# Kernel tuning notes

Measured on AMD Instinct MI355X. Metric: run time of the kernel, lower is better.

The kernel has to match this reference:

```python
import jax, jax.numpy as jnp
import numpy as np

HEAD_NUM = 16


def setup_inputs() -> dict:
    key = jax.random.key(0)
    k1, k2, k3, k4 = jax.random.split(key, 4)
    B, S, E = 8, 1024, 1024
    inputs = jax.random.normal(k1, (B, S, E), dtype=jnp.float32)
    W_Query = jax.random.normal(k2, (E, E), dtype=jnp.float32) * 0.05
    W_Key = jax.random.normal(k3, (E, E), dtype=jnp.float32) * 0.05
    W_Value = jax.random.normal(k4, (E, E), dtype=jnp.float32) * 0.05
    return {"inputs": inputs, "W_Query": W_Query, "W_Key": W_Key, "W_Value": W_Value}


def reference(inputs, W_Query, W_Key, W_Value):
    B, S, E = inputs.shape
    H = HEAD_NUM
    D = E // H
    # QKV projections: [B,S,E] @ [E,E] -> [B,S,E]
    q = jnp.einsum('bse,ef->bsf', inputs, W_Query).reshape(B, S, H, D)
    k = jnp.einsum('bse,ef->bsf', inputs, W_Key).reshape(B, S, H, D)
    v = jnp.einsum('bse,ef->bsf', inputs, W_Value).reshape(B, S, H, D)
    # NOTE: original has NO 1/sqrt(D) scaling.
    scores = jnp.einsum('bihd,bjhd->bhij', q, k)  # [B,H,S,S]
    att = jax.nn.softmax(scores, axis=-1)
    out = jnp.einsum('bhij,bjhd->bihd', att, v).reshape(B, S, E)
    return jax.nn.relu(out)
```

## Files before the change

### kernel.cpp

```cpp
#include <hip/hip_runtime.h>
#include <cstdint>
#include <cstddef>

#define B_ 8
#define S_ 1024
#define E_ 1024
#define H_ 16
#define D_ 64
#define M_ (B_*S_)

typedef _Float16 f16;
typedef __attribute__((ext_vector_type(8))) _Float16 f16x8;
typedef __attribute__((ext_vector_type(4))) _Float16 f16x4;
typedef __attribute__((ext_vector_type(4))) float  f32x4;
typedef __attribute__((ext_vector_type(16))) float f32x16;
typedef __attribute__((ext_vector_type(4))) int    int4v;
typedef __attribute__((ext_vector_type(2))) int    int2v;

__device__ __forceinline__ f32x4 mfma16(f16x8 a, f16x8 b, f32x4 c) {
  return __builtin_amdgcn_mfma_f32_16x16x32_f16(a, b, c, 0, 0, 0);
}
__device__ __forceinline__ f32x16 mfma32(f16x8 a, f16x8 b, f32x16 c) {
  return __builtin_amdgcn_mfma_f32_32x32x16_f16(a, b, c, 0, 0, 0);
}
__device__ __forceinline__ void gll16(const f16* g, f16* l) {
  __builtin_amdgcn_global_load_lds(
      (const __attribute__((address_space(1))) void*)g,
      (__attribute__((address_space(3))) void*)l, 16, 0, 0);
}
__device__ __forceinline__ int pkrtz(float lo, float hi) {
  return __builtin_bit_cast(int, __builtin_amdgcn_cvt_pkrtz(lo, hi));
}

__global__ __launch_bounds__(256) void prep_kernel(
    const float* __restrict__ X, const float* __restrict__ Wq,
    const float* __restrict__ Wk, const float* __restrict__ Wv,
    f16* __restrict__ Xf, f16* __restrict__ oq, f16* __restrict__ ok,
    f16* __restrict__ ov) {
  __shared__ float t[64][65];
  const int bid = blockIdx.x;
  if (bid < 4096) {
    size_t i = ((size_t)bid * 256 + threadIdx.x) * 8;
    f32x4 v0 = *(const f32x4*)&X[i];
    f32x4 v1 = *(const f32x4*)&X[i + 4];
    f16x8 hv;
#pragma unroll
    for (int j = 0; j < 4; ++j) {
      hv[j] = (f16)v0[j];
      hv[j + 4] = (f16)v1[j];
    }
    *(f16x8*)&Xf[i] = hv;
    return;
  }
  const int wid = bid - 4096;
  const int which = wid >> 8, tile = wid & 255;
  const float* W = which == 0 ? Wq : (which == 1 ? Wk : Wv);
  f16* o = which == 0 ? oq : (which == 1 ? ok : ov);
  const float scl = which == 0 ? 1.4426950408889634f : 1.0f;
  const int f0 = (tile & 15) * 64, e0 = (tile >> 4) * 64;
  const int tx = threadIdx.x & 63, tyy = threadIdx.x >> 6;
#pragma unroll
  for (int j = 0; j < 16; ++j) {
    int row = 4 * j + tyy;
    t[row][tx] = W[(size_t)(e0 + row) * E_ + f0 + tx];
  }
  __syncthreads();
#pragma unroll
  for (int j = 0; j < 16; ++j) {
    int row = 4 * j + tyy;
    o[(size_t)(f0 + row) * E_ + e0 + tx] = (f16)(t[tx][row] * scl);
  }
}

__global__ __launch_bounds__(256) void gemm_qkv_kernel(
    const f16* __restrict__ Xf,
    const f16* __restrict__ Wq, const f16* __restrict__ Wk,
    const f16* __restrict__ Wv,
    f16* __restrict__ Qf, f16* __restrict__ Kf, f16* __restrict__ Vt) {
  __shared__ f16 sA[128][64], sB[128][64];
  const int bid = blockIdx.x;
  const int xcd = bid & 7, idx = bid >> 3;
  const int mb = xcd * 8 + idx / 24;
  const int nb = idx % 24;
  const int z = nb >> 3;
  const int n0 = (nb & 7) * 128, m0 = mb * 128;
  const f16* __restrict__ Bt = z == 0 ? Wq : (z == 1 ? Wk : Wv);
  const int tid = threadIdx.x;
  const int lane = tid & 63, w = tid >> 6;
  const int wm = (w >> 1) * 64, wn = (w & 1) * 64;
  const int fr = lane & 15, fg = lane >> 4;
  f32x4 acc[4][4] = {};
  for (int k0 = 0; k0 < E_; k0 += 64) {
#pragma unroll
    for (int i = 0; i < 4; ++i) {
      int ci = tid + i * 256;
      int r = ci >> 3, cl = ci & 7;
      int cs = (cl ^ (r & 7)) * 8;
      gll16(Xf + (size_t)(m0 + r) * E_ + k0 + cs, &sA[0][0] + ci * 8);
      gll16(Bt + (size_t)(n0 + r) * E_ + k0 + cs, &sB[0][0] + ci * 8);
    }
    __syncthreads();
#pragma unroll
    for (int kh2 = 0; kh2 < 2; ++kh2) {
      f16x8 ah[4];
#pragma unroll
      for (int mi = 0; mi < 4; ++mi) {
        int rA = wm + mi * 16 + fr;
        ah[mi] = *(const f16x8*)&sA[rA][(((kh2 * 4 + fg) ^ (rA & 7))) * 8];
      }
#pragma unroll
      for (int ni = 0; ni < 4; ++ni) {
        int rB = wn + ni * 16 + fr;
        f16x8 bh = *(const f16x8*)&sB[rB][(((kh2 * 4 + fg) ^ (rB & 7))) * 8];
#pragma unroll
        for (int mi = 0; mi < 4; ++mi)
          acc[mi][ni] = mfma16(ah[mi], bh, acc[mi][ni]);
      }
    }
    __syncthreads();
  }
  if (z < 2) {
    f16* Of = z == 0 ? Qf : Kf;
#pragma unroll
    for (int mi = 0; mi < 4; ++mi)
#pragma unroll
      for (int ni = 0; ni < 4; ++ni)
#pragma unroll
        for (int r = 0; r < 4; ++r) {
          int row = m0 + wm + mi * 16 + (lane >> 4) * 4 + r;
          int col = n0 + wn + ni * 16 + fr;
          int bb = row >> 10, s = row & 1023;
          int hd = col >> 6, d = col & 63;
          Of[((size_t)(bb * H_ + hd) * S_ + s) * D_ + d] = (f16)acc[mi][ni][r];
        }
  } else {
#pragma unroll
    for (int mi = 0; mi < 4; ++mi)
#pragma unroll
      for (int ni = 0; ni < 4; ++ni) {
        int row = m0 + wm + mi * 16 + (lane >> 4) * 4;
        int col = n0 + wn + ni * 16 + fr;
        int bb = row >> 10, s = row & 1023;
        int hd = col >> 6, d = col & 63;
        f16x4 p;
#pragma unroll
        for (int r = 0; r < 4; ++r) p[r] = (f16)acc[mi][ni][r];
        *(f16x4*)&Vt[((size_t)(bb * H_ + hd) * D_ + d) * S_ + s] = p;
      }
  }
}

__global__ __launch_bounds__(256, 4) void attn_kernel(
    const f16* __restrict__ Qf, const f16* __restrict__ Kf,
    const f16* __restrict__ Vt, float* __restrict__ out) {
  __shared__ f16 sK[2][64][64], sV[2][64][64];
  const int bid = blockIdx.x;
  const int bh = (bid & 7) * 16 + (bid >> 6);
  const int qb = (bid >> 3) & 7;
  const int hd = bh & 15, bb = bh >> 4;
  const int tid = threadIdx.x;
  const int lane = tid & 63, w = tid >> 6;
  const int cq = lane & 31, h = lane >> 5;
  const int rsw = cq & 7;
  const size_t base = (size_t)bh * (S_ * D_);
  const f16* Qf_p = Qf + base;
  const f16* Kf_p = Kf + base;
  const f16* Vt_p = Vt + base;
  const int q0 = qb * 128 + w * 32;

  f16x8 qh_[4];
#pragma unroll
  for (int ks = 0; ks < 4; ++ks)
    qh_[ks] = *(const f16x8*)&Qf_p[(size_t)(q0 + cq) * D_ + ks * 16 + 8 * h];

  float m_run, l_run;
  f32x16 O[2] = {};
  f16x8 pf[4];

#define STAGE(buf, kb)                                                        \
  {                                                                           \
    _Pragma("unroll")                                                         \
    for (int half = 0; half < 2; ++half) {                                    \
      int ci = tid + half * 256;                                              \
      int row = ci >> 3, cl = ci & 7;                                         \
      int cs = cl ^ (row & 7);                                                \
      gll16(Kf_p + (size_t)((kb) + row) * D_ + cs * 8, &sK[buf][0][0] + ci * 8); \
      gll16(Vt_p + (size_t)row * S_ + (kb) + cs * 8, &sV[buf][0][0] + ci * 8);   \
    }                                                                         \
  }

#define QKT(scv, bufi)                                                        \
  {                                                                           \
    _Pragma("unroll")                                                         \
    for (int f = 0; f < 2; ++f) {                                             \
      _Pragma("unroll")                                                       \
      for (int ks = 0; ks < 4; ++ks) {                                        \
        int cc = ((2 * ks + h) ^ rsw) * 8;                                    \
        f16x8 kv = *(const f16x8*)&sK[bufi][f * 32 + cq][cc];                 \
        scv[f] = mfma32(kv, qh_[ks], scv[f]);                                 \
      }                                                                       \
    }                                                                         \
  }

#define MAXTREE(pm, scv)                                                      \
  {                                                                           \
    float t4[4];                                                              \
    _Pragma("unroll")                                                         \
    for (int i = 0; i < 4; ++i) {                                             \
      float a = fmaxf(fmaxf(scv[0][i], scv[0][i + 4]),                        \
                      fmaxf(scv[0][i + 8], scv[0][i + 12]));                  \
      float b = fmaxf(fmaxf(scv[1][i], scv[1][i + 4]),                        \
                      fmaxf(scv[1][i + 8], scv[1][i + 12]));                  \
      t4[i] = fmaxf(a, b);                                                    \
    }                                                                         \
    pm = fmaxf(fmaxf(t4[0], t4[1]), fmaxf(t4[2], t4[3]));                     \
    pm = fmaxf(pm, __shfl_xor(pm, 32));                                       \
  }

#define ROWSUM(rs, scv)                                                       \
  {                                                                           \
    float rs0 = 0.f, rs1 = 0.f, rs2 = 0.f, rs3 = 0.f;                         \
    _Pragma("unroll")                                                         \
    for (int f = 0; f < 2; ++f) {                                             \
      _Pragma("unroll")                                                       \
      for (int r4 = 0; r4 < 4; ++r4) {                                        \
        rs0 += scv[f][4 * r4 + 0];                                            \
        rs1 += scv[f][4 * r4 + 1];                                            \
        rs2 += scv[f][4 * r4 + 2];                                            \
        rs3 += scv[f][4 * r4 + 3];                                            \
      }                                                                       \
    }                                                                         \
    rs = (rs0 + rs1) + (rs2 + rs3);                                           \
    rs += __shfl_xor(rs, 32);                                                 \
  }

#define PFBUILD(scv)                                                          \
  {                                                                           \
    _Pragma("unroll")                                                         \
    for (int f = 0; f < 2; ++f) {                                             \
      _Pragma("unroll")                                                       \
      for (int ksl = 0; ksl < 2; ++ksl) {                                     \
        int b0 = 8 * ksl;                                                     \
        int a1 = pkrtz(scv[f][b0 + 0], scv[f][b0 + 1]);                       \
        int b1 = pkrtz(scv[f][b0 + 4], scv[f][b0 + 5]);                       \
        int2v r1 = __builtin_amdgcn_permlane32_swap(a1, b1, false, false);    \
        int a2 = pkrtz(scv[f][b0 + 2], scv[f][b0 + 3]);                       \
        int b2 = pkrtz(scv[f][b0 + 6], scv[f][b0 + 7]);                       \
        int2v r2 = __builtin_amdgcn_permlane32_swap(a2, b2, false, false);    \
        int4v wd;                                                             \
        wd[0] = r1[0]; wd[1] = r2[0]; wd[2] = r1[1]; wd[3] = r2[1];           \
        pf[2 * f + ksl] = __builtin_bit_cast(f16x8, wd);                      \
      }                                                                       \
    }                                                                         \
  }

#define PVT(bufi)                                                             \
  {                                                                           \
    _Pragma("unroll")                                                         \
    for (int ks = 0; ks < 4; ++ks) {                                          \
      int cc = ((2 * ks + h) ^ rsw) * 8;                                      \
      _Pragma("unroll")                                                       \
      for (int df = 0; df < 2; ++df) {                                        \
        f16x8 vf = *(const f16x8*)&sV[bufi][df * 32 + cq][cc];                \
        O[df] = mfma32(vf, pf[ks], O[df]);                                    \
      }                                                                       \
    }                                                                         \
  }

  STAGE(0, 0);
  asm volatile("s_waitcnt vmcnt(0)" ::: "memory");
  __builtin_amdgcn_sched_barrier(0);
  __builtin_amdgcn_s_barrier();
  STAGE(1, 64);
  {
    f32x16 sc[2] = {};
    __builtin_amdgcn_s_setprio(1);
    QKT(sc, 0);
    __builtin_amdgcn_s_setprio(0);
    float pm;
    MAXTREE(pm, sc);
    m_run = pm;
#pragma unroll
    for (int f = 0; f < 2; ++f)
#pragma unroll
      for (int r = 0; r < 16; ++r)
        sc[f][r] = __builtin_amdgcn_exp2f(sc[f][r] - pm);
    float rs;
    ROWSUM(rs, sc);
    l_run = rs;
    PFBUILD(sc);
    __builtin_amdgcn_s_setprio(1);
    PVT(0);
    __builtin_amdgcn_s_setprio(0);
  }
  asm volatile("s_waitcnt vmcnt(0)" ::: "memory");
  __builtin_amdgcn_sched_barrier(0);
  __builtin_amdgcn_s_barrier();

  for (int t = 1; t < 16; ++t) {
    const int cur = t & 1;
    if (t < 15) STAGE(cur ^ 1, (t + 1) * 64);

    f32x16 sc[2];
#pragma unroll
    for (int f = 0; f < 2; ++f)
#pragma unroll
      for (int r = 0; r < 16; ++r) sc[f][r] = -m_run;
    __builtin_amdgcn_s_setprio(1);
    QKT(sc, cur);
    __builtin_amdgcn_s_setprio(0);

#pragma unroll
    for (int f = 0; f < 2; ++f)
#pragma unroll
      for (int r = 0; r < 16; ++r)
        sc[f][r] = __builtin_amdgcn_exp2f(sc[f][r]);

    float pm;
    MAXTREE(pm, sc);
    if (__any(pm > 2048.f)) {
      float pmx = fmaxf(pm, 1.0f);
      float scl = 1.0f / pmx;
      m_run += __builtin_amdgcn_logf(pmx);
      l_run *= scl;
#pragma unroll
      for (int f = 0; f < 2; ++f)
#pragma unroll
        for (int r = 0; r < 16; ++r) sc[f][r] *= scl;
#pragma unroll
      for (int df = 0; df < 2; ++df)
#pragma unroll
        for (int i = 0; i < 16; ++i) O[df][i] *= scl;
    }

    float rs;
    ROWSUM(rs, sc);
    l_run += rs;
    PFBUILD(sc);
    __builtin_amdgcn_s_setprio(1);
    PVT(cur);
    __builtin_amdgcn_s_setprio(0);

    asm volatile("s_waitcnt vmcnt(0)" ::: "memory");
    __builtin_amdgcn_sched_barrier(0);
    __builtin_amdgcn_s_barrier();
  }

  float inv = 1.0f / l_run;
  int s = q0 + cq;
  float* orow = out + ((size_t)bb * S_ + s) * E_ + hd * 64;
#pragma unroll
  for (int df = 0; df < 2; ++df)
#pragma unroll
    for (int g = 0; g < 4; ++g) {
      f32x4 vv;
#pragma unroll
      for (int j = 0; j < 4; ++j)
        vv[j] = fmaxf(O[df][4 * g + j] * inv, 0.f);
      *(f32x4*)&orow[df * 32 + 8 * g + 4 * h] = vv;
    }
}

extern "C" void kernel_launch(void* const* d_in, const int* in_sizes, int n_in,
                              void* d_out, int out_size, void* d_ws, size_t ws_size,
                              hipStream_t stream) {
  const float* X  = (const float*)d_in[0];
  const float* Wq = (const float*)d_in[1];
  const float* Wk = (const float*)d_in[2];
  const float* Wv = (const float*)d_in[3];
  float* out = (float*)d_out;
  char* ws = (char*)d_ws;

  const size_t WSZ = (size_t)E_ * E_ * sizeof(f16);
  const size_t QSZ = (size_t)M_ * E_ * sizeof(f16);
  f16* Wqf = (f16*)(ws);
  f16* Wkf = (f16*)(ws + WSZ);
  f16* Wvf = (f16*)(ws + 2 * WSZ);
  char* p = ws + 3 * WSZ;
  f16* Xf = (f16*)(p);
  f16* Qf = (f16*)(p + QSZ);
  f16* Kf = (f16*)(p + 2 * QSZ);
  f16* Vt = (f16*)(p + 3 * QSZ);

  prep_kernel<<<4864, 256, 0, stream>>>(X, Wq, Wk, Wv, Xf, Wqf, Wkf, Wvf);

  gemm_qkv_kernel<<<1536, 256, 0, stream>>>(
      Xf, Wqf, Wkf, Wvf, Qf, Kf, Vt);

  attn_kernel<<<1024, 256, 0, stream>>>(Qf, Kf, Vt, out);
}
```

Measured before the change: 133.5 us.

## Concatenate QKV weights into 128x192 GEMM tiles and gate softmax rescale on row sum

The Q, K and V weights are stored as one concatenated matrix, so the QKV GEMM uses 128x192 tiles (1024 blocks instead of 1536). This gives more reuse of each loaded A tile and fewer total A loads, at the cost of more accumulator registers and LDS per block. In attention, the separate max-tree reduction before rescaling is removed. The overflow check now uses the row sum that is computed anyway, which cuts cross-lane reductions per KV tile.

```diff
diff --git a/kernel.cpp b/kernel.cpp
--- a/kernel.cpp
+++ b/kernel.cpp
@@ -35,8 +35,7 @@
 __global__ __launch_bounds__(256) void prep_kernel(
     const float* __restrict__ X, const float* __restrict__ Wq,
     const float* __restrict__ Wk, const float* __restrict__ Wv,
-    f16* __restrict__ Xf, f16* __restrict__ oq, f16* __restrict__ ok,
-    f16* __restrict__ ov) {
+    f16* __restrict__ Xf, f16* __restrict__ Wcat) {
   __shared__ float t[64][65];
   const int bid = blockIdx.x;
   if (bid < 4096) {
@@ -55,7 +54,7 @@
   const int wid = bid - 4096;
   const int which = wid >> 8, tile = wid & 255;
   const float* W = which == 0 ? Wq : (which == 1 ? Wk : Wv);
-  f16* o = which == 0 ? oq : (which == 1 ? ok : ov);
+  f16* o = Wcat + (size_t)which * E_ * E_;
   const float scl = which == 0 ? 1.4426950408889634f : 1.0f;
   const int f0 = (tile & 15) * 64, e0 = (tile >> 4) * 64;
   const int tx = threadIdx.x & 63, tyy = threadIdx.x >> 6;
@@ -73,23 +72,19 @@
 }
 
 __global__ __launch_bounds__(256) void gemm_qkv_kernel(
-    const f16* __restrict__ Xf,
-    const f16* __restrict__ Wq, const f16* __restrict__ Wk,
-    const f16* __restrict__ Wv,
+    const f16* __restrict__ Xf, const f16* __restrict__ Wcat,
     f16* __restrict__ Qf, f16* __restrict__ Kf, f16* __restrict__ Vt) {
-  __shared__ f16 sA[128][64], sB[128][64];
+  __shared__ f16 sA[128][64], sB[192][64];
   const int bid = blockIdx.x;
   const int xcd = bid & 7, idx = bid >> 3;
-  const int mb = xcd * 8 + idx / 24;
-  const int nb = idx % 24;
-  const int z = nb >> 3;
-  const int n0 = (nb & 7) * 128, m0 = mb * 128;
-  const f16* __restrict__ Bt = z == 0 ? Wq : (z == 1 ? Wk : Wv);
+  const int mb = xcd * 8 + (idx >> 4);
+  const int nb = idx & 15;
+  const int m0 = mb * 128, n0 = nb * 192;
   const int tid = threadIdx.x;
   const int lane = tid & 63, w = tid >> 6;
-  const int wm = (w >> 1) * 64, wn = (w & 1) * 64;
+  const int wm = (w >> 1) * 64, wn = (w & 1) * 96;
   const int fr = lane & 15, fg = lane >> 4;
-  f32x4 acc[4][4] = {};
+  f32x4 acc[4][6] = {};
   for (int k0 = 0; k0 < E_; k0 += 64) {
 #pragma unroll
     for (int i = 0; i < 4; ++i) {
@@ -97,7 +92,13 @@
       int r = ci >> 3, cl = ci & 7;
       int cs = (cl ^ (r & 7)) * 8;
       gll16(Xf + (size_t)(m0 + r) * E_ + k0 + cs, &sA[0][0] + ci * 8);
-      gll16(Bt + (size_t)(n0 + r) * E_ + k0 + cs, &sB[0][0] + ci * 8);
+    }
+#pragma unroll
+    for (int i = 0; i < 6; ++i) {
+      int ci = tid + i * 256;
+      int r = ci >> 3, cl = ci & 7;
+      int cs = (cl ^ (r & 7)) * 8;
+      gll16(Wcat + (size_t)(n0 + r) * E_ + k0 + cs, &sB[0][0] + ci * 8);
     }
     __syncthreads();
 #pragma unroll
@@ -109,7 +110,7 @@
         ah[mi] = *(const f16x8*)&sA[rA][(((kh2 * 4 + fg) ^ (rA & 7))) * 8];
       }
 #pragma unroll
-      for (int ni = 0; ni < 4; ++ni) {
+      for (int ni = 0; ni < 6; ++ni) {
         int rB = wn + ni * 16 + fr;
         f16x8 bh = *(const f16x8*)&sB[rB][(((kh2 * 4 + fg) ^ (rB & 7))) * 8];
 #pragma unroll
@@ -119,34 +120,32 @@
     }
     __syncthreads();
   }
-  if (z < 2) {
-    f16* Of = z == 0 ? Qf : Kf;
-#pragma unroll
-    for (int mi = 0; mi < 4; ++mi)
-#pragma unroll
-      for (int ni = 0; ni < 4; ++ni)
+#pragma unroll
+  for (int ni = 0; ni < 6; ++ni) {
+    int col = n0 + wn + ni * 16 + fr;
+    int z = col >> 10, cw = col & 1023;
+    int hd = cw >> 6, d = cw & 63;
+    if (z < 2) {
+      f16* Of = z == 0 ? Qf : Kf;
+#pragma unroll
+      for (int mi = 0; mi < 4; ++mi)
 #pragma unroll
         for (int r = 0; r < 4; ++r) {
-          int row = m0 + wm + mi * 16 + (lane >> 4) * 4 + r;
-          int col = n0 + wn + ni * 16 + fr;
+          int row = m0 + wm + mi * 16 + fg * 4 + r;
           int bb = row >> 10, s = row & 1023;
-          int hd = col >> 6, d = col & 63;
           Of[((size_t)(bb * H_ + hd) * S_ + s) * D_ + d] = (f16)acc[mi][ni][r];
         }
-  } else {
-#pragma unroll
-    for (int mi = 0; mi < 4; ++mi)
-#pragma unroll
-      for (int ni = 0; ni < 4; ++ni) {
-        int row = m0 + wm + mi * 16 + (lane >> 4) * 4;
-        int col = n0 + wn + ni * 16 + fr;
+    } else {
+#pragma unroll
+      for (int mi = 0; mi < 4; ++mi) {
+        int row = m0 + wm + mi * 16 + fg * 4;
         int bb = row >> 10, s = row & 1023;
-        int hd = col >> 6, d = col & 63;
         f16x4 p;
 #pragma unroll
         for (int r = 0; r < 4; ++r) p[r] = (f16)acc[mi][ni][r];
         *(f16x4*)&Vt[((size_t)(bb * H_ + hd) * D_ + d) * S_ + s] = p;
       }
+    }
   }
 }
 
@@ -316,26 +315,25 @@
       for (int r = 0; r < 16; ++r)
         sc[f][r] = __builtin_amdgcn_exp2f(sc[f][r]);
 
-    float pm;
-    MAXTREE(pm, sc);
-    if (__any(pm > 2048.f)) {
-      float pmx = fmaxf(pm, 1.0f);
-      float scl = 1.0f / pmx;
-      m_run += __builtin_amdgcn_logf(pmx);
-      l_run *= scl;
-#pragma unroll
-      for (int f = 0; f < 2; ++f)
-#pragma unroll
-        for (int r = 0; r < 16; ++r) sc[f][r] *= scl;
-#pragma unroll
-      for (int df = 0; df < 2; ++df)
-#pragma unroll
-        for (int i = 0; i < 16; ++i) O[df][i] *= scl;
-    }
-
     float rs;
     ROWSUM(rs, sc);
-    l_run += rs;
+    if (__any(rs > 2048.f)) {
+      float rsx = fmaxf(rs, 1.0f);
+      float scl = 1.0f / rsx;
+      m_run += __builtin_amdgcn_logf(rsx);
+      l_run = l_run * scl + rs * scl;
+#pragma unroll
+      for (int f = 0; f < 2; ++f)
+#pragma unroll
+        for (int r = 0; r < 16; ++r) sc[f][r] *= scl;
+#pragma unroll
+      for (int df = 0; df < 2; ++df)
+#pragma unroll
+        for (int i = 0; i < 16; ++i) O[df][i] *= scl;
+    } else {
+      l_run += rs;
+    }
+
     PFBUILD(sc);
     __builtin_amdgcn_s_setprio(1);
     PVT(cur);
@@ -373,19 +371,16 @@
 
   const size_t WSZ = (size_t)E_ * E_ * sizeof(f16);
   const size_t QSZ = (size_t)M_ * E_ * sizeof(f16);
-  f16* Wqf = (f16*)(ws);
-  f16* Wkf = (f16*)(ws + WSZ);
-  f16* Wvf = (f16*)(ws + 2 * WSZ);
+  f16* Wcat = (f16*)(ws);
   char* p = ws + 3 * WSZ;
   f16* Xf = (f16*)(p);
   f16* Qf = (f16*)(p + QSZ);
   f16* Kf = (f16*)(p + 2 * QSZ);
   f16* Vt = (f16*)(p + 3 * QSZ);
 
-  prep_kernel<<<4864, 256, 0, stream>>>(X, Wq, Wk, Wv, Xf, Wqf, Wkf, Wvf);
-
-  gemm_qkv_kernel<<<1536, 256, 0, stream>>>(
-      Xf, Wqf, Wkf, Wvf, Qf, Kf, Vt);
+  prep_kernel<<<4864, 256, 0, stream>>>(X, Wq, Wk, Wv, Xf, Wcat);
+
+  gemm_qkv_kernel<<<1024, 256, 0, stream>>>(Xf, Wcat, Qf, Kf, Vt);
 
   attn_kernel<<<1024, 256, 0, stream>>>(Qf, Kf, Vt, out);
 }
```

Result: slower. 251.4 us (+88.3%).
